# Kernel tuning notes

Measured on AMD Instinct MI355X. Metric: run time of the kernel, lower is better.

Reference implementation:

```python
import jax, jax.numpy as jnp
import numpy as np

B, P, E, D, A = 128, 49, 2048, 512, 512


def setup_inputs() -> dict:
    key = jax.random.key(0)
    ks = jax.random.split(key, 10)
    s = lambda k, shape, fan: jax.random.normal(k, shape, jnp.float32) * (1.0 / np.sqrt(fan))
    return {
        "encoder_out": jax.random.normal(ks[0], (B, P, E), jnp.float32),
        "decoder_hidden": jax.random.normal(ks[1], (B, D), jnp.float32),
        "We": s(ks[2], (A, E), E),  # encoder_att weight
        "be": jnp.zeros((A,), jnp.float32),
        "Wd": s(ks[3], (A, D), D),  # decoder_att weight
        "bd": jnp.zeros((A,), jnp.float32),
        "Wb": s(ks[4], (A, A, A), A),  # Bilinear weight [out,in1,in2]
        "bb": jnp.zeros((A,), jnp.float32),
        "Wf": s(ks[5], (1, A), A),  # full_att weight
        "bf": jnp.zeros((1,), jnp.float32),
    }


def reference(encoder_out, decoder_hidden, We, be, Wd, bd, Wb, bb, Wf, bf):
    # att1: [B,P,A]; att2: [B,A]
    att1 = jnp.einsum('bpe,ae->bpa', encoder_out, We) + be
    att2 = jnp.einsum('bd,ad->ba', decoder_hidden, Wd) + bd
    # nn.Bilinear(att1, att2_expanded): out[b,p,k] = sum_ij att1[b,p,i]*Wb[k,i,j]*att2[b,j] + bb[k]
    # contract att2 first since it is shared across the P=49 positions
    u = jnp.einsum('bj,kij->bki', att2, Wb)            # [B,A,A]
    bil = jnp.einsum('bpi,bki->bpk', att1, u) + bb     # [B,P,A]
    att = jnp.einsum('bpk,ok->bpo', jax.nn.relu(bil), Wf)[..., 0] + bf[0]  # [B,P]
    alpha = jax.nn.softmax(att, axis=1)                # [B,P]
    attention_weighted_encoding = jnp.einsum('bpe,bp->be', encoder_out, alpha)
    return (attention_weighted_encoding, alpha)
```

## Files before the change

kernel.cpp:

```cpp
#include <hip/hip_runtime.h>
#include <stdint.h>

typedef unsigned short ushort_t;
typedef float f32x4 __attribute__((ext_vector_type(4)));
typedef _Float16 half8 __attribute__((ext_vector_type(8)));

#define DEVFN static __device__ __forceinline__

DEVFN ushort_t cvt_f16(float f) {
  union { _Float16 h; ushort_t u; } v;
  v.h = (_Float16)f;
  return v.u;
}

DEVFN half8 cvt_frag(f32x4 a, f32x4 b) {
  half8 r;
  r[0] = (_Float16)a[0]; r[1] = (_Float16)a[1];
  r[2] = (_Float16)a[2]; r[3] = (_Float16)a[3];
  r[4] = (_Float16)b[0]; r[5] = (_Float16)b[1];
  r[6] = (_Float16)b[2]; r[7] = (_Float16)b[3];
  return r;
}

DEVFN void gload16(const void* g, void* lds) {
  __builtin_amdgcn_global_load_lds(
      (const __attribute__((address_space(1))) uint32_t*)g,
      (__attribute__((address_space(3))) uint32_t*)lds, 16, 0, 0);
}

__global__ __launch_bounds__(256) void k_att2(
    const float* __restrict__ dec, const float* __restrict__ Wd,
    const float* __restrict__ bd, ushort_t* __restrict__ att2) {
  __shared__ __align__(16) float ds[512];
  int b = blockIdx.x, t = threadIdx.x;
  ds[t] = dec[b * 512 + t];
  ds[t + 256] = dec[b * 512 + t + 256];
  __syncthreads();
  for (int o = 0; o < 2; ++o) {
    int a = o * 256 + t;
    const f32x4* wr = (const f32x4*)(Wd + (size_t)a * 512);
    const f32x4* dr = (const f32x4*)ds;
    f32x4 acc = {0.f, 0.f, 0.f, 0.f};
#pragma unroll 8
    for (int k4 = 0; k4 < 128; ++k4) acc += wr[k4] * dr[k4];
    float s = bd[a] + acc[0] + acc[1] + acc[2] + acc[3];
    att2[b * 512 + a] = cvt_f16(s);
  }
}

__global__ __launch_bounds__(256) void k_att1(
    const float* __restrict__ A, const float* __restrict__ B,
    const float* __restrict__ bias, ushort_t* __restrict__ C) {
  __shared__ __align__(16) float As[128 * 64];
  __shared__ __align__(16) float Bs[128 * 64];
  const int t = threadIdx.x, w = t >> 6, l = t & 63;
  const int wm = w >> 1, wn = w & 1;
  const int m0 = blockIdx.y * 128, n0 = blockIdx.x * 128;
  f32x4 acc[4][4] = {};
  for (int ks = 0; ks < 32; ++ks) {
    const int k0 = ks * 64;
#pragma unroll
    for (int i = 0; i < 8; ++i) {
      int Lb = i * 256 + (w << 6);
      int L = Lb + l, r = L >> 4, s = L & 15, gc = s ^ (r & 15);
      gload16((const char*)(A + (size_t)(m0 + r) * 2048 + k0) + gc * 16,
              (char*)As + (size_t)Lb * 16);
    }
#pragma unroll
    for (int i = 0; i < 8; ++i) {
      int Lb = i * 256 + (w << 6);
      int L = Lb + l, r = L >> 4, s = L & 15, gc = s ^ (r & 15);
      gload16((const char*)(B + (size_t)(n0 + r) * 2048 + k0) + gc * 16,
              (char*)Bs + (size_t)Lb * 16);
    }
    __syncthreads();
    const int q = l >> 4, lm = l & 15;
#pragma unroll
    for (int ksub = 0; ksub < 2; ++ksub) {
      half8 af[4], bfr[4];
#pragma unroll
      for (int mi = 0; mi < 4; ++mi) {
        int r = wm * 64 + mi * 16 + lm;
        int d0 = ksub * 8 + q * 2;
        f32x4 v0 = *(const f32x4*)((const char*)As + ((size_t)r * 16 + (d0 ^ (r & 15))) * 16);
        f32x4 v1 = *(const f32x4*)((const char*)As + ((size_t)r * 16 + ((d0 + 1) ^ (r & 15))) * 16);
        af[mi] = cvt_frag(v0, v1);
      }
#pragma unroll
      for (int ni = 0; ni < 4; ++ni) {
        int r = wn * 64 + ni * 16 + lm;
        int d0 = ksub * 8 + q * 2;
        f32x4 v0 = *(const f32x4*)((const char*)Bs + ((size_t)r * 16 + (d0 ^ (r & 15))) * 16);
        f32x4 v1 = *(const f32x4*)((const char*)Bs + ((size_t)r * 16 + ((d0 + 1) ^ (r & 15))) * 16);
        bfr[ni] = cvt_frag(v0, v1);
      }
#pragma unroll
      for (int mi = 0; mi < 4; ++mi)
#pragma unroll
        for (int ni = 0; ni < 4; ++ni)
          acc[mi][ni] = __builtin_amdgcn_mfma_f32_16x16x32_f16(af[mi], bfr[ni], acc[mi][ni], 0, 0, 0);
    }
    __syncthreads();
  }
  const int q = l >> 4, lm = l & 15;
  for (int mi = 0; mi < 4; ++mi)
    for (int ni = 0; ni < 4; ++ni)
      for (int rg = 0; rg < 4; ++rg) {
        int m = m0 + wm * 64 + mi * 16 + q * 4 + rg;
        int n = n0 + wn * 64 + ni * 16 + lm;
        C[(size_t)m * 512 + n] = cvt_f16(acc[mi][ni][rg] + bias[n]);
      }
}

__global__ __launch_bounds__(256) void k_u(
    const ushort_t* __restrict__ att2, const float* __restrict__ Wb,
    ushort_t* __restrict__ u) {
  __shared__ __align__(16) ushort_t As[128 * 64];
  __shared__ __align__(16) float Bs[128 * 64];
  const int t = threadIdx.x, w = t >> 6, l = t & 63;
  const int wm = w >> 1, wn = w & 1;
  const int n0 = blockIdx.x * 128;
  f32x4 acc[4][4] = {};
  for (int ks = 0; ks < 8; ++ks) {
    const int j0 = ks * 64;
#pragma unroll
    for (int i = 0; i < 4; ++i) {
      int Lb = i * 256 + (w << 6);
      int L = Lb + l, r = L >> 3, s = L & 7, gc = s ^ (r & 7);
      gload16((const char*)(att2 + (size_t)r * 512 + j0) + gc * 16,
              (char*)As + (size_t)Lb * 16);
    }
#pragma unroll
    for (int i = 0; i < 8; ++i) {
      int Lb = i * 256 + (w << 6);
      int L = Lb + l, r = L >> 4, s = L & 15, gc = s ^ (r & 15);
      gload16((const char*)(Wb + (size_t)(n0 + r) * 512 + j0) + gc * 16,
              (char*)Bs + (size_t)Lb * 16);
    }
    __syncthreads();
    const int q = l >> 4, lm = l & 15;
#pragma unroll
    for (int ksub = 0; ksub < 2; ++ksub) {
      half8 af[4], bfr[4];
#pragma unroll
      for (int mi = 0; mi < 4; ++mi) {
        int r = wm * 64 + mi * 16 + lm;
        int d = ksub * 4 + q;
        af[mi] = *(const half8*)((const char*)As + ((size_t)r * 8 + (d ^ (r & 7))) * 16);
      }
#pragma unroll
      for (int ni = 0; ni < 4; ++ni) {
        int r = wn * 64 + ni * 16 + lm;
        int d0 = ksub * 8 + q * 2;
        f32x4 v0 = *(const f32x4*)((const char*)Bs + ((size_t)r * 16 + (d0 ^ (r & 15))) * 16);
        f32x4 v1 = *(const f32x4*)((const char*)Bs + ((size_t)r * 16 + ((d0 + 1) ^ (r & 15))) * 16);
        bfr[ni] = cvt_frag(v0, v1);
      }
#pragma unroll
      for (int mi = 0; mi < 4; ++mi)
#pragma unroll
        for (int ni = 0; ni < 4; ++ni)
          acc[mi][ni] = __builtin_amdgcn_mfma_f32_16x16x32_f16(af[mi], bfr[ni], acc[mi][ni], 0, 0, 0);
    }
    __syncthreads();
  }
  const int q = l >> 4, lm = l & 15;
  for (int mi = 0; mi < 4; ++mi)
    for (int ni = 0; ni < 4; ++ni)
      for (int rg = 0; rg < 4; ++rg) {
        int b = wm * 64 + mi * 16 + q * 4 + rg;
        int n = n0 + wn * 64 + ni * 16 + lm;
        u[(size_t)b * 262144 + n] = cvt_f16(acc[mi][ni][rg]);
      }
}

__global__ __launch_bounds__(256) void k_bil(
    const ushort_t* __restrict__ att1, const ushort_t* __restrict__ u,
    const float* __restrict__ bb, const float* __restrict__ Wf,
    float* __restrict__ att) {
  __shared__ __align__(16) ushort_t As[64 * 64];
  __shared__ __align__(16) ushort_t Bs[128 * 64];
  const int t = threadIdx.x, w = t >> 6, l = t & 63;
  const int wm = w >> 1, wn = w & 1;
  const int b = blockIdx.x, kq = blockIdx.y;
  const ushort_t* Arow = att1 + (size_t)b * 49 * 512;
  const ushort_t* Brow = u + (size_t)b * 262144 + (size_t)kq * 128 * 512;
  f32x4 acc[2][4] = {};
  for (int ks = 0; ks < 8; ++ks) {
    const int i0 = ks * 64;
#pragma unroll
    for (int i = 0; i < 2; ++i) {
      int Lb = i * 256 + (w << 6);
      int L = Lb + l, r = L >> 3, s = L & 7, gc = s ^ (r & 7);
      gload16((const char*)(Arow + (size_t)r * 512 + i0) + gc * 16,
              (char*)As + (size_t)Lb * 16);
    }
#pragma unroll
    for (int i = 0; i < 4; ++i) {
      int Lb = i * 256 + (w << 6);
      int L = Lb + l, r = L >> 3, s = L & 7, gc = s ^ (r & 7);
      gload16((const char*)(Brow + (size_t)r * 512 + i0) + gc * 16,
              (char*)Bs + (size_t)Lb * 16);
    }
    __syncthreads();
    const int q = l >> 4, lm = l & 15;
#pragma unroll
    for (int ksub = 0; ksub < 2; ++ksub) {
      half8 af[2], bfr[4];
#pragma unroll
      for (int mi = 0; mi < 2; ++mi) {
        int r = wm * 32 + mi * 16 + lm;
        int d = ksub * 4 + q;
        af[mi] = *(const half8*)((const char*)As + ((size_t)r * 8 + (d ^ (r & 7))) * 16);
      }
#pragma unroll
      for (int ni = 0; ni < 4; ++ni) {
        int r = wn * 64 + ni * 16 + lm;
        int d = ksub * 4 + q;
        bfr[ni] = *(const half8*)((const char*)Bs + ((size_t)r * 8 + (d ^ (r & 7))) * 16);
      }
#pragma unroll
      for (int mi = 0; mi < 2; ++mi)
#pragma unroll
        for (int ni = 0; ni < 4; ++ni)
          acc[mi][ni] = __builtin_amdgcn_mfma_f32_16x16x32_f16(af[mi], bfr[ni], acc[mi][ni], 0, 0, 0);
    }
    __syncthreads();
  }
  const int q = l >> 4, lm = l & 15;
#pragma unroll
  for (int mi = 0; mi < 2; ++mi) {
#pragma unroll
    for (int rg = 0; rg < 4; ++rg) {
      float s = 0.f;
#pragma unroll
      for (int ni = 0; ni < 4; ++ni) {
        int k = kq * 128 + wn * 64 + ni * 16 + lm;
        float v = acc[mi][ni][rg] + bb[k];
        s += fmaxf(v, 0.f) * Wf[k];
      }
      s += __shfl_xor(s, 1);
      s += __shfl_xor(s, 2);
      s += __shfl_xor(s, 4);
      s += __shfl_xor(s, 8);
      int p = wm * 32 + mi * 16 + q * 4 + rg;
      if (lm == 0 && p < 49) atomicAdd(att + b * 49 + p, s);
    }
  }
}

__global__ __launch_bounds__(64) void k_softmax(
    const float* __restrict__ att, float* __restrict__ alpha) {
  int b = blockIdx.x, l = threadIdx.x;
  float x = (l < 49) ? att[b * 49 + l] : -1e30f;
  float m = x;
  for (int off = 32; off; off >>= 1) m = fmaxf(m, __shfl_xor(m, off));
  float e = (l < 49) ? __expf(x - m) : 0.f;
  float s = e;
  for (int off = 32; off; off >>= 1) s += __shfl_xor(s, off);
  if (l < 49) alpha[b * 49 + l] = e / s;
}

__global__ __launch_bounds__(256) void k_awe(
    const float* __restrict__ enc, const float* __restrict__ alpha,
    float* __restrict__ awe) {
  __shared__ float al[49];
  int b = blockIdx.y, h = blockIdx.x, t = threadIdx.x;
  if (t < 49) al[t] = alpha[b * 49 + t];
  __syncthreads();
  int e4 = h * 256 + t;
  const f32x4* ep = (const f32x4*)(enc + (size_t)b * 49 * 2048) + e4;
  f32x4 acc = {0.f, 0.f, 0.f, 0.f};
#pragma unroll 7
  for (int p = 0; p < 49; ++p) acc += al[p] * ep[(size_t)p * 512];
  ((f32x4*)(awe + (size_t)b * 2048))[e4] = acc;
}

extern "C" void kernel_launch(void* const* d_in, const int* in_sizes, int n_in,
                              void* d_out, int out_size, void* d_ws, size_t ws_size,
                              hipStream_t stream) {
  (void)in_sizes; (void)n_in; (void)out_size; (void)ws_size;
  const float* enc = (const float*)d_in[0];
  const float* dec = (const float*)d_in[1];
  const float* We  = (const float*)d_in[2];
  const float* be  = (const float*)d_in[3];
  const float* Wd  = (const float*)d_in[4];
  const float* bd  = (const float*)d_in[5];
  const float* Wb  = (const float*)d_in[6];
  const float* bb  = (const float*)d_in[7];
  const float* Wf  = (const float*)d_in[8];

  char* ws = (char*)d_ws;
  ushort_t* att2 = (ushort_t*)ws;
  ushort_t* att1 = (ushort_t*)(ws + 131072);
  ushort_t* u    = (ushort_t*)(ws + 6619136);
  float*    att  = (float*)(ws + 73728000);

  float* awe   = (float*)d_out;
  float* alpha = (float*)d_out + 262144;

  hipMemsetAsync(att, 0, 128 * 49 * sizeof(float), stream);
  k_att2<<<dim3(128), 256, 0, stream>>>(dec, Wd, bd, att2);
  k_att1<<<dim3(4, 49), 256, 0, stream>>>(enc, We, be, att1);
  k_u<<<dim3(2048), 256, 0, stream>>>(att2, Wb, u);
  k_bil<<<dim3(128, 4), 256, 0, stream>>>(att1, u, bb, Wf, att);
  k_softmax<<<dim3(128), 64, 0, stream>>>(att, alpha);
  k_awe<<<dim3(2, 128), 256, 0, stream>>>(enc, alpha, awe);
}
```

Before: 858.7 us.

## Pre-convert encoder and We to fp16, shrink att1 tiles, fuse softmax into awe

```diff
diff --git a/kernel.cpp b/kernel.cpp
--- a/kernel.cpp
+++ b/kernel.cpp
@@ -4,6 +4,7 @@
 typedef unsigned short ushort_t;
 typedef float f32x4 __attribute__((ext_vector_type(4)));
 typedef _Float16 half8 __attribute__((ext_vector_type(8)));
+typedef ushort_t u16x4 __attribute__((ext_vector_type(4)));
 
 #define DEVFN static __device__ __forceinline__
 
@@ -26,6 +27,25 @@
   __builtin_amdgcn_global_load_lds(
       (const __attribute__((address_space(1))) uint32_t*)g,
       (__attribute__((address_space(3))) uint32_t*)lds, 16, 0, 0);
+}
+
+__global__ __launch_bounds__(256) void k_prep(
+    const float* __restrict__ enc, const float* __restrict__ We,
+    ushort_t* __restrict__ encf16, ushort_t* __restrict__ Wef16) {
+  const int NQ_ENC = 3211264;
+  const int NQ_TOT = 3473408;
+  int idx = blockIdx.x * 256 + threadIdx.x;
+  int stride = gridDim.x * 256;
+  for (int q = idx; q < NQ_TOT; q += stride) {
+    const float* src; ushort_t* dst; int j;
+    if (q < NQ_ENC) { src = enc; dst = encf16; j = q; }
+    else            { src = We;  dst = Wef16;  j = q - NQ_ENC; }
+    f32x4 v = ((const f32x4*)src)[j];
+    u16x4 o;
+    o[0] = cvt_f16(v[0]); o[1] = cvt_f16(v[1]);
+    o[2] = cvt_f16(v[2]); o[3] = cvt_f16(v[3]);
+    ((u16x4*)dst)[j] = o;
+  }
 }
 
 __global__ __launch_bounds__(256) void k_att2(
@@ -49,27 +69,27 @@
 }
 
 __global__ __launch_bounds__(256) void k_att1(
-    const float* __restrict__ A, const float* __restrict__ B,
+    const ushort_t* __restrict__ A, const ushort_t* __restrict__ B,
     const float* __restrict__ bias, ushort_t* __restrict__ C) {
-  __shared__ __align__(16) float As[128 * 64];
-  __shared__ __align__(16) float Bs[128 * 64];
+  __shared__ __align__(16) ushort_t As[64 * 64];
+  __shared__ __align__(16) ushort_t Bs[128 * 64];
   const int t = threadIdx.x, w = t >> 6, l = t & 63;
   const int wm = w >> 1, wn = w & 1;
-  const int m0 = blockIdx.y * 128, n0 = blockIdx.x * 128;
-  f32x4 acc[4][4] = {};
+  const int m0 = blockIdx.y * 64, n0 = blockIdx.x * 128;
+  f32x4 acc[2][4] = {};
   for (int ks = 0; ks < 32; ++ks) {
     const int k0 = ks * 64;
 #pragma unroll
-    for (int i = 0; i < 8; ++i) {
-      int Lb = i * 256 + (w << 6);
-      int L = Lb + l, r = L >> 4, s = L & 15, gc = s ^ (r & 15);
+    for (int i = 0; i < 2; ++i) {
+      int Lb = i * 256 + (w << 6);
+      int L = Lb + l, r = L >> 3, s = L & 7, gc = s ^ (r & 7);
       gload16((const char*)(A + (size_t)(m0 + r) * 2048 + k0) + gc * 16,
               (char*)As + (size_t)Lb * 16);
     }
 #pragma unroll
-    for (int i = 0; i < 8; ++i) {
-      int Lb = i * 256 + (w << 6);
-      int L = Lb + l, r = L >> 4, s = L & 15, gc = s ^ (r & 15);
+    for (int i = 0; i < 4; ++i) {
+      int Lb = i * 256 + (w << 6);
+      int L = Lb + l, r = L >> 3, s = L & 7, gc = s ^ (r & 7);
       gload16((const char*)(B + (size_t)(n0 + r) * 2048 + k0) + gc * 16,
               (char*)Bs + (size_t)Lb * 16);
     }
@@ -77,25 +97,21 @@
     const int q = l >> 4, lm = l & 15;
 #pragma unroll
     for (int ksub = 0; ksub < 2; ++ksub) {
-      half8 af[4], bfr[4];
-#pragma unroll
-      for (int mi = 0; mi < 4; ++mi) {
-        int r = wm * 64 + mi * 16 + lm;
-        int d0 = ksub * 8 + q * 2;
-        f32x4 v0 = *(const f32x4*)((const char*)As + ((size_t)r * 16 + (d0 ^ (r & 15))) * 16);
-        f32x4 v1 = *(const f32x4*)((const char*)As + ((size_t)r * 16 + ((d0 + 1) ^ (r & 15))) * 16);
-        af[mi] = cvt_frag(v0, v1);
+      half8 af[2], bfr[4];
+#pragma unroll
+      for (int mi = 0; mi < 2; ++mi) {
+        int r = wm * 32 + mi * 16 + lm;
+        int d = ksub * 4 + q;
+        af[mi] = *(const half8*)((const char*)As + ((size_t)r * 8 + (d ^ (r & 7))) * 16);
       }
 #pragma unroll
       for (int ni = 0; ni < 4; ++ni) {
         int r = wn * 64 + ni * 16 + lm;
-        int d0 = ksub * 8 + q * 2;
-        f32x4 v0 = *(const f32x4*)((const char*)Bs + ((size_t)r * 16 + (d0 ^ (r & 15))) * 16);
-        f32x4 v1 = *(const f32x4*)((const char*)Bs + ((size_t)r * 16 + ((d0 + 1) ^ (r & 15))) * 16);
-        bfr[ni] = cvt_frag(v0, v1);
-      }
-#pragma unroll
-      for (int mi = 0; mi < 4; ++mi)
+        int d = ksub * 4 + q;
+        bfr[ni] = *(const half8*)((const char*)Bs + ((size_t)r * 8 + (d ^ (r & 7))) * 16);
+      }
+#pragma unroll
+      for (int mi = 0; mi < 2; ++mi)
 #pragma unroll
         for (int ni = 0; ni < 4; ++ni)
           acc[mi][ni] = __builtin_amdgcn_mfma_f32_16x16x32_f16(af[mi], bfr[ni], acc[mi][ni], 0, 0, 0);
@@ -103,10 +119,10 @@
     __syncthreads();
   }
   const int q = l >> 4, lm = l & 15;
-  for (int mi = 0; mi < 4; ++mi)
+  for (int mi = 0; mi < 2; ++mi)
     for (int ni = 0; ni < 4; ++ni)
       for (int rg = 0; rg < 4; ++rg) {
-        int m = m0 + wm * 64 + mi * 16 + q * 4 + rg;
+        int m = m0 + wm * 32 + mi * 16 + q * 4 + rg;
         int n = n0 + wn * 64 + ni * 16 + lm;
         C[(size_t)m * 512 + n] = cvt_f16(acc[mi][ni][rg] + bias[n]);
       }
@@ -249,24 +265,24 @@
   }
 }
 
-__global__ __launch_bounds__(64) void k_softmax(
-    const float* __restrict__ att, float* __restrict__ alpha) {
-  int b = blockIdx.x, l = threadIdx.x;
-  float x = (l < 49) ? att[b * 49 + l] : -1e30f;
-  float m = x;
-  for (int off = 32; off; off >>= 1) m = fmaxf(m, __shfl_xor(m, off));
-  float e = (l < 49) ? __expf(x - m) : 0.f;
-  float s = e;
-  for (int off = 32; off; off >>= 1) s += __shfl_xor(s, off);
-  if (l < 49) alpha[b * 49 + l] = e / s;
-}
-
 __global__ __launch_bounds__(256) void k_awe(
-    const float* __restrict__ enc, const float* __restrict__ alpha,
-    float* __restrict__ awe) {
+    const float* __restrict__ enc, const float* __restrict__ att,
+    float* __restrict__ awe, float* __restrict__ alpha) {
   __shared__ float al[49];
   int b = blockIdx.y, h = blockIdx.x, t = threadIdx.x;
-  if (t < 49) al[t] = alpha[b * 49 + t];
+  if (t < 64) {
+    float x = (t < 49) ? att[b * 49 + t] : -1e30f;
+    float m = x;
+    for (int off = 32; off; off >>= 1) m = fmaxf(m, __shfl_xor(m, off));
+    float e = (t < 49) ? __expf(x - m) : 0.f;
+    float s = e;
+    for (int off = 32; off; off >>= 1) s += __shfl_xor(s, off);
+    if (t < 49) {
+      float a = e / s;
+      al[t] = a;
+      if (h == 0) alpha[b * 49 + t] = a;
+    }
+  }
   __syncthreads();
   int e4 = h * 256 + t;
   const f32x4* ep = (const f32x4*)(enc + (size_t)b * 49 * 2048) + e4;
@@ -291,19 +307,21 @@
   const float* Wf  = (const float*)d_in[8];
 
   char* ws = (char*)d_ws;
-  ushort_t* att2 = (ushort_t*)ws;
-  ushort_t* att1 = (ushort_t*)(ws + 131072);
-  ushort_t* u    = (ushort_t*)(ws + 6619136);
-  float*    att  = (float*)(ws + 73728000);
+  ushort_t* att2   = (ushort_t*)ws;
+  ushort_t* att1   = (ushort_t*)(ws + 131072);
+  ushort_t* u      = (ushort_t*)(ws + 6619136);
+  float*    att    = (float*)(ws + 73728000);
+  ushort_t* encf16 = (ushort_t*)(ws + 73753088);
+  ushort_t* Wef16  = (ushort_t*)(ws + 99443200);
 
   float* awe   = (float*)d_out;
   float* alpha = (float*)d_out + 262144;
 
   hipMemsetAsync(att, 0, 128 * 49 * sizeof(float), stream);
+  k_prep<<<dim3(2048), 256, 0, stream>>>(enc, We, encf16, Wef16);
   k_att2<<<dim3(128), 256, 0, stream>>>(dec, Wd, bd, att2);
-  k_att1<<<dim3(4, 49), 256, 0, stream>>>(enc, We, be, att1);
+  k_att1<<<dim3(4, 98), 256, 0, stream>>>(encf16, Wef16, be, att1);
   k_u<<<dim3(2048), 256, 0, stream>>>(att2, Wb, u);
   k_bil<<<dim3(128, 4), 256, 0, stream>>>(att1, u, bb, Wf, att);
-  k_softmax<<<dim3(128), 64, 0, stream>>>(att, alpha);
-  k_awe<<<dim3(2, 128), 256, 0, stream>>>(enc, alpha, awe);
-}
+  k_awe<<<dim3(2, 128), 256, 0, stream>>>(enc, att, awe, alpha);
+}
```

Result: faster. 828.5 us (-3.5%).
